# Performance work log

Measured on AMD Instinct MI355X. Metric: run time of the kernel, lower is better.

The kernel has to match this reference:

```python
import jax, jax.numpy as jnp
import numpy as np
from jax import lax

DIM = 256
HEADS = 8
C3 = DIM * 3 // 4  # 192
C1 = DIM // 4      # 64


def conv1x1(x, w):
    # x: [b,c,h,w], w: [o,c] (1x1 conv, no bias)
    return jnp.einsum('bchw,oc->bohw', x, w)


def dwconv3x3(x, w):
    # x: [b,c,h,w], w: [c,1,3,3] depthwise
    return lax.conv_general_dilated(
        x, w, window_strides=(1, 1), padding='SAME',
        feature_group_count=x.shape[1],
        dimension_numbers=('NCHW', 'OIHW', 'NCHW'))


def l2norm(x, eps=1e-12):
    # torch F.normalize: x / max(||x||, eps) along last dim
    n = jnp.sqrt(jnp.sum(x * x, axis=-1, keepdims=True))
    return x / jnp.maximum(n, eps)


def setup_inputs() -> dict:
    key = jax.random.key(0)
    ks = jax.random.split(key, 10)
    s = 0.02
    return {
        'x': jax.random.normal(ks[0], (4, DIM, 128, 128), jnp.float32),
        'k_v': jax.random.normal(ks[1], (4, 256), jnp.float32),
        'temperature': jnp.ones((HEADS, 1, 1), jnp.float32),
        'w_kR': jax.random.normal(ks[2], (C3, 192), jnp.float32) * s,
        'w_kI': jax.random.normal(ks[3], (C1, 64), jnp.float32) * s,
        'w_qR': jax.random.normal(ks[4], (DIM, C3), jnp.float32) * s,
        'w_qdw': jax.random.normal(ks[5], (DIM, 1, 3, 3), jnp.float32) * s,
        'w_kvI': jax.random.normal(ks[6], (2 * DIM, C1), jnp.float32) * s,
        'w_kvdw': jax.random.normal(ks[7], (2 * DIM, 1, 3, 3), jnp.float32) * s,
        'w_proj': jax.random.normal(ks[8], (DIM, DIM), jnp.float32) * s,
    }


def reference(x, k_v, temperature, w_kR, w_kI, w_qR, w_qdw, w_kvI, w_kvdw, w_proj):
    b, c, h, w = x.shape
    # FiLM-style modulation: x * kv + x
    kvr = (k_v[:, :192] @ w_kR.T)[:, :, None, None]  # [b, C3, 1, 1]
    kvi = (k_v[:, 192:] @ w_kI.T)[:, :, None, None]  # [b, C1, 1, 1]
    x_r = x[:, :C3] * kvr + x[:, :C3]
    x_i = x[:, C3:] * kvi + x[:, C3:]
    # QKV projections
    q = dwconv3x3(conv1x1(x_r, w_qR), w_qdw)          # [b, dim, h, w]
    kv = dwconv3x3(conv1x1(x_i, w_kvI), w_kvdw)       # [b, 2*dim, h, w]
    k, v = jnp.split(kv, 2, axis=1)
    hd = DIM // HEADS
    hw = h * w
    q = q.reshape(b, HEADS, hd, hw)
    k = k.reshape(b, HEADS, hd, hw)
    v = v.reshape(b, HEADS, hd, hw)
    # channel-wise (transposed) attention with L2 norm + temperature
    q = l2norm(q)
    k = l2norm(k)
    attn = jnp.einsum('bhcn,bhdn->bhcd', q, k) * temperature  # [b,H,hd,hd]
    attn = jax.nn.softmax(attn, axis=-1)
    out = jnp.einsum('bhcd,bhdn->bhcn', attn, v)
    out = out.reshape(b, DIM, h, w)
    return conv1x1(out, w_proj)
```

## Files before the change

### kernel.cpp

```cpp
#include <hip/hip_runtime.h>
#include <math.h>

#define HW 16384

typedef unsigned int uint;
typedef short bfrag __attribute__((ext_vector_type(8)));
typedef float f32x4 __attribute__((ext_vector_type(4)));

union FragCvt { uint4 u; bfrag v; };

__device__ inline uint pack2bf(float a, float b) {
  uint ua = __builtin_bit_cast(uint, a);
  uint ub = __builtin_bit_cast(uint, b);
  ua = (ua + 0x7FFFu + ((ua >> 16) & 1u)) >> 16;
  ub = (ub + 0x7FFFu + ((ub >> 16) & 1u)) & 0xFFFF0000u;
  return ua | ub;
}

__device__ inline void cvt_hilo(float4 a, float4 b, bfrag& hi, bfrag& lo) {
  float v0[8] = {a.x, a.y, a.z, a.w, b.x, b.y, b.z, b.w};
  uint hv[4], lv[4];
  #pragma unroll
  for (int i = 0; i < 4; ++i) {
    float x0 = v0[2 * i], x1 = v0[2 * i + 1];
    uint h = pack2bf(x0, x1);
    float h0 = __builtin_bit_cast(float, h << 16);
    float h1 = __builtin_bit_cast(float, h & 0xFFFF0000u);
    hv[i] = h;
    lv[i] = pack2bf(x0 - h0, x1 - h1);
  }
  FragCvt ch, cl;
  ch.u = make_uint4(hv[0], hv[1], hv[2], hv[3]);
  cl.u = make_uint4(lv[0], lv[1], lv[2], lv[3]);
  hi = ch.v;
  lo = cl.v;
}

__global__ __launch_bounds__(256) void mod_kernel(
    const float* __restrict__ kv, const float* __restrict__ wkR,
    const float* __restrict__ wkI, float* __restrict__ mod)
{
  int b = blockIdx.x;
  int c = threadIdx.x;
  const float* kvb = kv + b * 256;
  float s = 0.f;
  if (c < 192) {
    const float* wr = wkR + c * 192;
    for (int j = 0; j < 192; ++j) s += kvb[j] * wr[j];
  } else {
    const float* wi = wkI + (c - 192) * 64;
    for (int j = 0; j < 64; ++j) s += kvb[192 + j] * wi[j];
  }
  mod[b * 256 + c] = 1.f + s;
}

__device__ __forceinline__ void mgemm_body(
    const float* __restrict__ Wt, int ldW,
    const float* __restrict__ Xt,
    const float* __restrict__ modc,
    float* __restrict__ Yt,
    int K, int t, unsigned short* Al, unsigned short* Bl, float* Ml)
{
  int w = t >> 6, l = t & 63;
  int wm = (w >> 1) * 64, wn = (w & 1) * 64;
  int lm = l & 15, lk = (l >> 4) * 8;

  int am = t >> 1, ako = (t & 1) * 16;
  int bn = t & 127, bo = (t >> 7) * 8;

  Ml[t] = (modc && t < K) ? modc[t] : 1.f;

  f32x4 acc[4][4];
  #pragma unroll
  for (int fi = 0; fi < 4; ++fi)
    #pragma unroll
    for (int fj = 0; fj < 4; ++fj) acc[fi][fj] = {0.f, 0.f, 0.f, 0.f};

  float xr[2][8];
  auto load_x = [&](int k0) {
    #pragma unroll
    for (int i = 0; i < 2; ++i) {
      int kb = k0 + bo + i * 16;
      #pragma unroll
      for (int r = 0; r < 8; ++r)
        xr[i][r] = Xt[(size_t)(kb + r) * HW + bn];
    }
  };

  load_x(0);

  for (int k0 = 0; k0 < K; k0 += 32) {
    __syncthreads();

    {
      const float* wsrc = Wt + (size_t)am * ldW + k0 + ako;
      float4 a0 = *(const float4*)(wsrc);
      float4 a1 = *(const float4*)(wsrc + 4);
      float4 a2 = *(const float4*)(wsrc + 8);
      float4 a3 = *(const float4*)(wsrc + 12);
      uint4 aw0, aw1;
      aw0.x = pack2bf(a0.x, a0.y); aw0.y = pack2bf(a0.z, a0.w);
      aw0.z = pack2bf(a1.x, a1.y); aw0.w = pack2bf(a1.z, a1.w);
      aw1.x = pack2bf(a2.x, a2.y); aw1.y = pack2bf(a2.z, a2.w);
      aw1.z = pack2bf(a3.x, a3.y); aw1.w = pack2bf(a3.z, a3.w);
      *(uint4*)&Al[am * 40 + ako] = aw0;
      *(uint4*)&Al[am * 40 + ako + 8] = aw1;
    }

    #pragma unroll
    for (int i = 0; i < 2; ++i) {
      float4 m0 = *(const float4*)&Ml[k0 + bo + i * 16];
      float4 m1 = *(const float4*)&Ml[k0 + bo + i * 16 + 4];
      uint4 bw;
      bw.x = pack2bf(xr[i][0] * m0.x, xr[i][1] * m0.y);
      bw.y = pack2bf(xr[i][2] * m0.z, xr[i][3] * m0.w);
      bw.z = pack2bf(xr[i][4] * m1.x, xr[i][5] * m1.y);
      bw.w = pack2bf(xr[i][6] * m1.z, xr[i][7] * m1.w);
      *(uint4*)&Bl[bn * 40 + bo + i * 16] = bw;
    }

    __syncthreads();

    bfrag af[4], bfr[4];
    #pragma unroll
    for (int fj = 0; fj < 4; ++fj) {
      FragCvt cv;
      cv.u = *(const uint4*)&Al[(wm + fj * 16 + lm) * 40 + lk];
      af[fj] = cv.v;
    }
    #pragma unroll
    for (int fi = 0; fi < 4; ++fi) {
      FragCvt cv;
      cv.u = *(const uint4*)&Bl[(wn + fi * 16 + lm) * 40 + lk];
      bfr[fi] = cv.v;
    }

    if (k0 + 32 < K) load_x(k0 + 32);

    #pragma unroll
    for (int fi = 0; fi < 4; ++fi)
      #pragma unroll
      for (int fj = 0; fj < 4; ++fj)
        acc[fi][fj] = __builtin_amdgcn_mfma_f32_16x16x32_bf16(
            bfr[fi], af[fj], acc[fi][fj], 0, 0, 0);
  }

  int ph = (l >> 4) * 4;
  #pragma unroll
  for (int fi = 0; fi < 4; ++fi)
    #pragma unroll
    for (int fj = 0; fj < 4; ++fj)
      *(f32x4*)&Yt[(size_t)(wm + fj * 16 + lm) * HW + wn + fi * 16 + ph] =
          acc[fi][fj];
}

__global__ __launch_bounds__(256, 4) void mgemm(
    const float* __restrict__ W, int ldW, size_t Wbstride,
    const float* __restrict__ X, int c0, size_t Xbstride,
    const float* __restrict__ mod,
    float* __restrict__ Y, size_t Ybstride, int K)
{
  __shared__ unsigned short Al[128 * 40];
  __shared__ unsigned short Bl[128 * 40];
  __shared__ float Ml[256];
  int b = blockIdx.z, mt = blockIdx.y, nt = blockIdx.x;
  mgemm_body(W + (size_t)b * Wbstride + (size_t)mt * 128 * ldW, ldW,
             X + (size_t)b * Xbstride + (size_t)c0 * HW + nt * 128,
             mod ? mod + b * 256 + c0 : (const float*)nullptr,
             Y + (size_t)b * Ybstride + (size_t)mt * 128 * HW + nt * 128,
             K, threadIdx.x, Al, Bl, Ml);
}

__global__ __launch_bounds__(256, 4) void mgemm_qk(
    const float* __restrict__ wqR, const float* __restrict__ wkvI,
    const float* __restrict__ X, const float* __restrict__ mod,
    float* __restrict__ Yq, float* __restrict__ Yk)
{
  __shared__ unsigned short Al[128 * 40];
  __shared__ unsigned short Bl[128 * 40];
  __shared__ float Ml[256];
  int b = blockIdx.z, mt = blockIdx.y, nt = blockIdx.x;
  if (mt < 2) {
    mgemm_body(wqR + (size_t)mt * 128 * 192, 192,
               X + (size_t)b * 4194304 + nt * 128,
               mod + b * 256,
               Yq + (size_t)b * 4194304 + (size_t)mt * 128 * HW + nt * 128,
               192, threadIdx.x, Al, Bl, Ml);
  } else {
    int m2 = mt - 2;
    mgemm_body(wkvI + (size_t)m2 * 128 * 64, 64,
               X + (size_t)b * 4194304 + (size_t)192 * HW + nt * 128,
               mod + b * 256 + 192,
               Yk + (size_t)b * 4194304 + (size_t)m2 * 128 * HW + nt * 128,
               64, threadIdx.x, Al, Bl, Ml);
  }
}

__global__ __launch_bounds__(256) void dwconv_kernel(
    const float* __restrict__ in, size_t in_bstride,
    const float* __restrict__ wdw,
    float* __restrict__ out, size_t out_bstride,
    float* __restrict__ ssq)
{
  int c = blockIdx.x;
  int b = blockIdx.y;
  int t = threadIdx.x;
  int r = t >> 5;
  int xq = t & 31;

  const float4* ip4 = (const float4*)(in + (size_t)b * in_bstride + ((size_t)c << 14));
  float4* op4 = (float4*)(out + (size_t)b * out_bstride + ((size_t)c << 14));
  const float* wp = wdw + c * 9;
  float w0 = wp[0], w1 = wp[1], w2 = wp[2], w3 = wp[3], w4 = wp[4],
        w5 = wp[5], w6 = wp[6], w7 = wp[7], w8 = wp[8];

  const float4 z4 = make_float4(0.f, 0.f, 0.f, 0.f);
  int y0 = r << 4;

  float4 a = (y0 > 0) ? ip4[((y0 - 1) << 5) + xq] : z4;
  float4 bb = ip4[(y0 << 5) + xq];

  float aL = __shfl_up(a.w, 1);  if (xq == 0)  aL = 0.f;
  float aR = __shfl_down(a.x, 1); if (xq == 31) aR = 0.f;
  float bL = __shfl_up(bb.w, 1); if (xq == 0)  bL = 0.f;
  float bR = __shfl_down(bb.x, 1); if (xq == 31) bR = 0.f;

  float ss = 0.f;
  #pragma unroll
  for (int i = 0; i < 16; ++i) {
    int y = y0 + i;
    int yc = (y + 1 < 128) ? (y + 1) : 127;
    float4 cc = ip4[(yc << 5) + xq];
    if (y + 1 >= 128) { cc.x = 0.f; cc.y = 0.f; cc.z = 0.f; cc.w = 0.f; }
    float cL = __shfl_up(cc.w, 1);  if (xq == 0)  cL = 0.f;
    float cR = __shfl_down(cc.x, 1); if (xq == 31) cR = 0.f;

    float4 o;
    o.x = w0 * aL  + w1 * a.x + w2 * a.y +
          w3 * bL  + w4 * bb.x + w5 * bb.y +
          w6 * cL  + w7 * cc.x + w8 * cc.y;
    o.y = w0 * a.x + w1 * a.y + w2 * a.z +
          w3 * bb.x + w4 * bb.y + w5 * bb.z +
          w6 * cc.x + w7 * cc.y + w8 * cc.z;
    o.z = w0 * a.y + w1 * a.z + w2 * a.w +
          w3 * bb.y + w4 * bb.z + w5 * bb.w +
          w6 * cc.y + w7 * cc.z + w8 * cc.w;
    o.w = w0 * a.z + w1 * a.w + w2 * aR +
          w3 * bb.z + w4 * bb.w + w5 * bR +
          w6 * cc.z + w7 * cc.w + w8 * cR;

    op4[(y << 5) + xq] = o;
    ss += o.x * o.x + o.y * o.y + o.z * o.z + o.w * o.w;

    a = bb; aL = bL; aR = bR;
    bb = cc; bL = cL; bR = cR;
  }

  if (ssq) {
    #pragma unroll
    for (int off = 32; off > 0; off >>= 1) ss += __shfl_down(ss, off);
    __shared__ float red[4];
    if ((t & 63) == 0) red[t >> 6] = ss;
    __syncthreads();
    if (t == 0) ssq[b * 256 + c] = red[0] + red[1] + red[2] + red[3];
  }
}

__global__ __launch_bounds__(256) void gram_kernel(
    const float* __restrict__ qdw, const float* __restrict__ kdw,
    float* __restrict__ S)
{
  int chunk = blockIdx.x, h = blockIdx.y, b = blockIdx.z;
  int t = threadIdx.x;
  int w = t >> 6, l = t & 63;
  int lm = l & 15;
  int lk8 = (l >> 4) * 8;

  const float* qh = qdw + (((size_t)b * 256 + h * 32) << 14);
  const float* kh = kdw + (((size_t)b * 256 + h * 32) << 14);
  const float* q0 = qh + ((size_t)lm << 14);
  const float* q1 = q0 + ((size_t)16 << 14);
  const float* k0 = kh + ((size_t)lm << 14);
  const float* k1 = k0 + ((size_t)16 << 14);

  int px0 = chunk * 1024 + w * 256 + lk8;

  f32x4 acc[2][2], accl[2][2];
  #pragma unroll
  for (int mi = 0; mi < 2; ++mi)
    #pragma unroll
    for (int nj = 0; nj < 2; ++nj) {
      acc[mi][nj] = {0.f, 0.f, 0.f, 0.f};
      accl[mi][nj] = {0.f, 0.f, 0.f, 0.f};
    }

  #pragma unroll 2
  for (int s = 0; s < 8; ++s) {
    int px = px0 + s * 32;
    float4 a0 = *(const float4*)(q0 + px);
    float4 a1 = *(const float4*)(q0 + px + 4);
    float4 a2 = *(const float4*)(q1 + px);
    float4 a3 = *(const float4*)(q1 + px + 4);
    float4 b0 = *(const float4*)(k0 + px);
    float4 b1 = *(const float4*)(k0 + px + 4);
    float4 b2 = *(const float4*)(k1 + px);
    float4 b3 = *(const float4*)(k1 + px + 4);

    bfrag qhF[2], qlF[2], khF[2], klF[2];
    cvt_hilo(a0, a1, qhF[0], qlF[0]);
    cvt_hilo(a2, a3, qhF[1], qlF[1]);
    cvt_hilo(b0, b1, khF[0], klF[0]);
    cvt_hilo(b2, b3, khF[1], klF[1]);

    #pragma unroll
    for (int mi = 0; mi < 2; ++mi)
      #pragma unroll
      for (int nj = 0; nj < 2; ++nj) {
        acc[mi][nj] = __builtin_amdgcn_mfma_f32_16x16x32_bf16(
            qhF[mi], khF[nj], acc[mi][nj], 0, 0, 0);
        accl[mi][nj] = __builtin_amdgcn_mfma_f32_16x16x32_bf16(
            qhF[mi], klF[nj], accl[mi][nj], 0, 0, 0);
        accl[mi][nj] = __builtin_amdgcn_mfma_f32_16x16x32_bf16(
            qlF[mi], khF[nj], accl[mi][nj], 0, 0, 0);
      }
  }

  __shared__ float red[4][1024];
  int orow = (l >> 4) * 4;
  #pragma unroll
  for (int mi = 0; mi < 2; ++mi)
    #pragma unroll
    for (int nj = 0; nj < 2; ++nj)
      #pragma unroll
      for (int r = 0; r < 4; ++r)
        red[w][(mi * 16 + orow + r) * 32 + nj * 16 + lm] =
            acc[mi][nj][r] + accl[mi][nj][r];
  __syncthreads();
  float* Sp = S + (((size_t)b * 8 + h) << 10);
  for (int idx = t; idx < 1024; idx += 256)
    atomicAdd(&Sp[idx], red[0][idx] + red[1][idx] + red[2][idx] + red[3][idx]);
}

__global__ __launch_bounds__(64) void softmax_kernel(
    float* __restrict__ S, const float* __restrict__ ssq,
    const float* __restrict__ ssk, const float* __restrict__ temp)
{
  int bh = blockIdx.x;
  int b = bh >> 3, h = bh & 7;
  int c = threadIdx.x;
  if (c >= 32) return;
  float* row = S + ((size_t)bh << 10) + c * 32;
  float invq = 1.f / fmaxf(sqrtf(ssq[b * 256 + h * 32 + c]), 1e-12f);
  float T = temp[h];
  float lg[32];
  float mx = -1e30f;
  for (int d = 0; d < 32; ++d) {
    float invk = 1.f / fmaxf(sqrtf(ssk[b * 256 + h * 32 + d]), 1e-12f);
    float v = row[d] * invq * invk * T;
    lg[d] = v;
    mx = fmaxf(mx, v);
  }
  float sum = 0.f;
  for (int d = 0; d < 32; ++d) { float e = expf(lg[d] - mx); lg[d] = e; sum += e; }
  float inv = 1.f / sum;
  for (int d = 0; d < 32; ++d) row[d] = lg[d] * inv;
}

__global__ __launch_bounds__(256) void mbuild_kernel(
    const float* __restrict__ attn, const float* __restrict__ wproj,
    float* __restrict__ M)
{
  int o = blockIdx.x, b = blockIdx.y;
  int col = threadIdx.x;
  int h = col >> 5, d = col & 31;
  const float* a = attn + (((size_t)b * 8 + h) << 10);
  const float* wp = wproj + o * 256 + h * 32;
  float s = 0.f;
  #pragma unroll
  for (int cc = 0; cc < 32; ++cc) s += wp[cc] * a[cc * 32 + d];
  M[((size_t)b * 256 + o) * 256 + col] = s;
}

extern "C" void kernel_launch(void* const* d_in, const int* in_sizes, int n_in,
                              void* d_out, int out_size, void* d_ws, size_t ws_size,
                              hipStream_t stream)
{
  const float* x      = (const float*)d_in[0];
  const float* k_v    = (const float*)d_in[1];
  const float* temp   = (const float*)d_in[2];
  const float* w_kR   = (const float*)d_in[3];
  const float* w_kI   = (const float*)d_in[4];
  const float* w_qR   = (const float*)d_in[5];
  const float* w_qdw  = (const float*)d_in[6];
  const float* w_kvI  = (const float*)d_in[7];
  const float* w_kvdw = (const float*)d_in[8];
  const float* w_proj = (const float*)d_in[9];
  float* out = (float*)d_out;

  float* ws   = (float*)d_ws;
  float* bufA = ws;
  float* bufB = ws + 16777216;
  float* bufC = ws + 33554432;
  float* sm   = ws + 50331648;
  float* mod  = sm;
  float* ssq  = sm + 1024;
  float* ssk  = sm + 2048;
  float* S    = sm + 3072;
  float* M    = sm + 3072 + 32768;

  hipMemsetAsync(S, 0, (size_t)32768 * sizeof(float), stream);

  mod_kernel<<<dim3(4), dim3(256), 0, stream>>>(k_v, w_kR, w_kI, mod);

  mgemm_qk<<<dim3(128, 4, 4), dim3(256), 0, stream>>>(
      w_qR, w_kvI, x, mod, bufA, bufB);

  dwconv_kernel<<<dim3(256, 4), dim3(256), 0, stream>>>(
      bufB, 4194304, w_kvdw, bufC, 4194304, ssk);

  dwconv_kernel<<<dim3(256, 4), dim3(256), 0, stream>>>(
      bufA, 4194304, w_qdw, bufB, 4194304, ssq);

  gram_kernel<<<dim3(16, 8, 4), dim3(256), 0, stream>>>(bufB, bufC, S);

  mgemm<<<dim3(128, 2, 4), dim3(256), 0, stream>>>(
      w_kvI + 256 * 64, 64, 0, x, 192, 4194304, mod, bufA, 4194304, 64);

  softmax_kernel<<<dim3(32), dim3(64), 0, stream>>>(S, ssq, ssk, temp);
  mbuild_kernel<<<dim3(256, 4), dim3(256), 0, stream>>>(S, w_proj, M);

  dwconv_kernel<<<dim3(256, 4), dim3(256), 0, stream>>>(
      bufA, 4194304, w_kvdw + 256 * 9, bufC, 4194304, (float*)nullptr);

  mgemm<<<dim3(128, 2, 4), dim3(256), 0, stream>>>(
      M, 256, 65536, bufC, 0, 4194304, (const float*)nullptr, out, 4194304, 256);
}
```

Before: 321.8 us.

## Double-buffer X and W register prefetch in mgemm body, relax launch bounds

Restructures the GEMM main loop to unroll by two K-steps, keeping two register buffers of X and prefetching W into registers one step ahead, so global loads for later steps overlap the current MFMA work. Launch bounds are relaxed from 4 to 2 blocks per SM to make room for the extra registers. This trades occupancy for deeper prefetch. The loop now assumes K is a multiple of 64 (192 and 64 are).

```diff
diff --git a/kernel.cpp b/kernel.cpp
--- a/kernel.cpp
+++ b/kernel.cpp
@@ -76,51 +76,48 @@
     #pragma unroll
     for (int fj = 0; fj < 4; ++fj) acc[fi][fj] = {0.f, 0.f, 0.f, 0.f};
 
-  float xr[2][8];
-  auto load_x = [&](int k0) {
+  float xrA[16], xrB[16];
+  float4 wv0, wv1, wv2, wv3;
+
+  auto load_x = [&](float* xr, int k0) {
     #pragma unroll
     for (int i = 0; i < 2; ++i) {
       int kb = k0 + bo + i * 16;
       #pragma unroll
       for (int r = 0; r < 8; ++r)
-        xr[i][r] = Xt[(size_t)(kb + r) * HW + bn];
+        xr[i * 8 + r] = Xt[(size_t)(kb + r) * HW + bn];
     }
   };
-
-  load_x(0);
-
-  for (int k0 = 0; k0 < K; k0 += 32) {
-    __syncthreads();
-
-    {
-      const float* wsrc = Wt + (size_t)am * ldW + k0 + ako;
-      float4 a0 = *(const float4*)(wsrc);
-      float4 a1 = *(const float4*)(wsrc + 4);
-      float4 a2 = *(const float4*)(wsrc + 8);
-      float4 a3 = *(const float4*)(wsrc + 12);
-      uint4 aw0, aw1;
-      aw0.x = pack2bf(a0.x, a0.y); aw0.y = pack2bf(a0.z, a0.w);
-      aw0.z = pack2bf(a1.x, a1.y); aw0.w = pack2bf(a1.z, a1.w);
-      aw1.x = pack2bf(a2.x, a2.y); aw1.y = pack2bf(a2.z, a2.w);
-      aw1.z = pack2bf(a3.x, a3.y); aw1.w = pack2bf(a3.z, a3.w);
-      *(uint4*)&Al[am * 40 + ako] = aw0;
-      *(uint4*)&Al[am * 40 + ako + 8] = aw1;
-    }
-
+  auto load_w = [&](int k0) {
+    const float* wsrc = Wt + (size_t)am * ldW + k0 + ako;
+    wv0 = *(const float4*)(wsrc);
+    wv1 = *(const float4*)(wsrc + 4);
+    wv2 = *(const float4*)(wsrc + 8);
+    wv3 = *(const float4*)(wsrc + 12);
+  };
+  auto pack_a = [&]() {
+    uint4 aw0, aw1;
+    aw0.x = pack2bf(wv0.x, wv0.y); aw0.y = pack2bf(wv0.z, wv0.w);
+    aw0.z = pack2bf(wv1.x, wv1.y); aw0.w = pack2bf(wv1.z, wv1.w);
+    aw1.x = pack2bf(wv2.x, wv2.y); aw1.y = pack2bf(wv2.z, wv2.w);
+    aw1.z = pack2bf(wv3.x, wv3.y); aw1.w = pack2bf(wv3.z, wv3.w);
+    *(uint4*)&Al[am * 40 + ako] = aw0;
+    *(uint4*)&Al[am * 40 + ako + 8] = aw1;
+  };
+  auto pack_b = [&](const float* xr, int k0) {
     #pragma unroll
     for (int i = 0; i < 2; ++i) {
       float4 m0 = *(const float4*)&Ml[k0 + bo + i * 16];
       float4 m1 = *(const float4*)&Ml[k0 + bo + i * 16 + 4];
       uint4 bw;
-      bw.x = pack2bf(xr[i][0] * m0.x, xr[i][1] * m0.y);
-      bw.y = pack2bf(xr[i][2] * m0.z, xr[i][3] * m0.w);
-      bw.z = pack2bf(xr[i][4] * m1.x, xr[i][5] * m1.y);
-      bw.w = pack2bf(xr[i][6] * m1.z, xr[i][7] * m1.w);
+      bw.x = pack2bf(xr[i * 8 + 0] * m0.x, xr[i * 8 + 1] * m0.y);
+      bw.y = pack2bf(xr[i * 8 + 2] * m0.z, xr[i * 8 + 3] * m0.w);
+      bw.z = pack2bf(xr[i * 8 + 4] * m1.x, xr[i * 8 + 5] * m1.y);
+      bw.w = pack2bf(xr[i * 8 + 6] * m1.z, xr[i * 8 + 7] * m1.w);
       *(uint4*)&Bl[bn * 40 + bo + i * 16] = bw;
     }
-
-    __syncthreads();
-
+  };
+  auto mfma_step = [&]() {
     bfrag af[4], bfr[4];
     #pragma unroll
     for (int fj = 0; fj < 4; ++fj) {
@@ -134,15 +131,34 @@
       cv.u = *(const uint4*)&Bl[(wn + fi * 16 + lm) * 40 + lk];
       bfr[fi] = cv.v;
     }
-
-    if (k0 + 32 < K) load_x(k0 + 32);
-
     #pragma unroll
     for (int fi = 0; fi < 4; ++fi)
       #pragma unroll
       for (int fj = 0; fj < 4; ++fj)
         acc[fi][fj] = __builtin_amdgcn_mfma_f32_16x16x32_bf16(
             bfr[fi], af[fj], acc[fi][fj], 0, 0, 0);
+  };
+
+  load_x(xrA, 0);
+  load_x(xrB, 32);
+  load_w(0);
+
+  for (int k0 = 0; k0 < K; k0 += 64) {
+    __syncthreads();
+    pack_a();
+    if (k0 + 32 < K) load_w(k0 + 32);
+    pack_b(xrA, k0);
+    if (k0 + 64 < K) load_x(xrA, k0 + 64);
+    __syncthreads();
+    mfma_step();
+
+    __syncthreads();
+    pack_a();
+    if (k0 + 64 < K) load_w(k0 + 64);
+    pack_b(xrB, k0 + 32);
+    if (k0 + 96 < K) load_x(xrB, k0 + 96);
+    __syncthreads();
+    mfma_step();
   }
 
   int ph = (l >> 4) * 4;
@@ -154,7 +170,7 @@
           acc[fi][fj];
 }
 
-__global__ __launch_bounds__(256, 4) void mgemm(
+__global__ __launch_bounds__(256, 2) void mgemm(
     const float* __restrict__ W, int ldW, size_t Wbstride,
     const float* __restrict__ X, int c0, size_t Xbstride,
     const float* __restrict__ mod,
@@ -171,7 +187,7 @@
              K, threadIdx.x, Al, Bl, Ml);
 }
 
-__global__ __launch_bounds__(256, 4) void mgemm_qk(
+__global__ __launch_bounds__(256, 2) void mgemm_qk(
     const float* __restrict__ wqR, const float* __restrict__ wkvI,
     const float* __restrict__ X, const float* __restrict__ mod,
     float* __restrict__ Yq, float* __restrict__ Yk)
```

Result: slower. 329.6 us (+2.4%).
